# Performance work log

Measured on AMD Instinct MI355X. Metric: run time of the kernel, lower is better.

Reference implementation:

```python
import jax, jax.numpy as jnp
import numpy as np

C0 = 0.28209479177387814
C1 = 0.4886025119029199
C2 = (1.0925484305920792, -1.0925484305920792, 0.31539156525252005,
      -1.0925484305920792, 0.5462742152960396)
EPS = 1e-6


def eval_sh_bases2(d):
    # d: [..., 3] unit directions -> [..., 9] SH basis (degree 2, svox2 convention)
    x, y, z = d[..., 0], d[..., 1], d[..., 2]
    return jnp.stack([
        jnp.full_like(x, C0),
        -C1 * y, C1 * z, -C1 * x,
        C2[0] * x * y, C2[1] * y * z,
        C2[2] * (2.0 * z * z - x * x - y * y),
        C2[3] * x * z, C2[4] * (x * x - y * y),
    ], axis=-1)


def get_sh_vals(xyz, sh_feats, invs, locs):
    # xyz: [N,3]; sh_feats: [J,9]; invs: [J,4,4]; locs: [J,3] -> weights [N,J]
    n = xyz.shape[0]
    xyz_h = jnp.concatenate([xyz, jnp.ones((n, 1), xyz.dtype)], axis=-1)  # [N,4]
    pts = jnp.einsum('jab,nb->jna', invs, xyz_h)[..., :3]  # [J,N,3]
    vd = locs[:, None, :] - pts                             # [J,N,3]
    norm = jnp.linalg.norm(vd, axis=-1)                     # [J,N]
    lengths = jnp.nan_to_num(norm)
    vd = vd / jnp.maximum(norm, 1e-12)[..., None]           # F.normalize
    sh = eval_sh_bases2(vd)                                 # [J,N,9]
    rads = jax.nn.relu(jnp.einsum('jnk,jk->jn', sh, sh_feats) + 0.5)
    rel = jax.nn.relu(1.0 - lengths / jnp.maximum(rads, EPS))
    rel = jnp.where(rads < EPS, 0.0, rel)
    return rel.T  # [N,J]


def weighted_transformation(pts, weights, transforms):
    # pts: [M,3]; weights: [M,J]; transforms: [J,4,4] (already inverse transforms,
    # if_transform_is_inv=True). Linear-blend the matrices and apply.
    wsum = weights.sum(axis=-1, keepdims=True)              # [M,1]
    wn = weights / jnp.maximum(wsum, EPS)
    T = jnp.einsum('mj,jab->mab', wn, transforms)           # [M,4,4]
    p_h = jnp.concatenate([pts, jnp.ones((pts.shape[0], 1), pts.dtype)], axis=-1)
    out = jnp.einsum('mab,mb->ma', T, p_h)[:, :3]
    return jnp.where(wsum > EPS, out, pts)                  # untouched if no weight


def setup_inputs() -> dict:
    key = jax.random.key(0)
    ks = jax.random.split(key, 5)
    B, S, J = 4096, 128, 24
    return {
        'xyz_sampled': jax.random.normal(ks[0], (B, S, 3), jnp.float32),
        'viewdirs': jax.random.normal(ks[1], (B, S, 3), jnp.float32),
        'transforms': jax.random.normal(ks[2], (J, 4, 4), jnp.float32),
        'ray_valid': jnp.ones((B, S), dtype=bool),
        'sh_feats': jax.random.normal(ks[3], (J, 9), jnp.float32),
        'locs': jax.random.normal(ks[4], (J, 3), jnp.float32),
    }


def reference(xyz_sampled, viewdirs, transforms, ray_valid, sh_feats, locs):
    shape = xyz_sampled.shape
    x = xyz_sampled.reshape(-1, 3)
    n = x.shape[0]
    tmp = jnp.concatenate([x, (xyz_sampled - viewdirs).reshape(-1, 3)], axis=0)  # [2N,3]
    w = get_sh_vals(x, sh_feats, transforms, locs)          # [N,J]
    w2 = jnp.concatenate([w, w], axis=0)                    # [2N,J]
    tmp = weighted_transformation(tmp, w2, transforms)      # [2N,3]
    xyz_out = tmp[:n]
    view_out = xyz_out - tmp[n:]
    return xyz_out.reshape(shape), view_out.reshape(shape)
```

## Files before the change

### kernel.cpp

```cpp
#include <hip/hip_runtime.h>

#define EPS 1e-6f
#define J 24


__global__ __launch_bounds__(256, 4) void shcaster_kernel(
    const float* __restrict__ xyz,
    const float* __restrict__ vdir,
    const float* __restrict__ transforms,
    const float* __restrict__ sh_feats,
    const float* __restrict__ locs,
    float* __restrict__ out,
    int n)
{
    __shared__ float4 sj[J][7];
    const int tid = threadIdx.x;

    if (tid < J) {
        const int j = tid;
        float F[9];
        #pragma unroll
        for (int k = 0; k < 9; ++k) F[k] = sh_feats[j * 9 + k];

        const float C0  = 0.28209479177387814f;
        const float C1  = 0.4886025119029199f;
        const float C2a = 1.0925484305920792f;

        const float f0  = C0 * F[0] + 0.5f;
        const float cy  = -C1 * F[1];
        const float cz  =  C1 * F[2];
        const float cx  = -C1 * F[3];
        const float cxy =  C2a * F[4];
        const float cyz = -C2a * F[5];
        const float c6  = 0.31539156525252005f * F[6];
        const float cxz = -C2a * F[7];
        const float c8  = 0.5462742152960396f  * F[8];

        float* s = (float*)&sj[j][0];
        #pragma unroll
        for (int k = 0; k < 12; ++k) s[k] = transforms[j * 16 + k];
        s[12] = locs[j * 3 + 0];
        s[13] = locs[j * 3 + 1];
        s[14] = locs[j * 3 + 2];
        s[15] = f0;
        s[16] = cx;  s[17] = cy;  s[18] = cz;  s[19] = cxy;
        s[20] = cyz; s[21] = cxz;
        s[22] = c8 - c6;
        s[23] = -c6 - c8;
        s[24] = 2.0f * c6;
        s[25] = 0.f; s[26] = 0.f; s[27] = 0.f;
    }
    __syncthreads();

    const int i = blockIdx.x * blockDim.x + tid;
    if (i >= n) return;

    const float px = xyz[3 * i + 0];
    const float py = xyz[3 * i + 1];
    const float pz = xyz[3 * i + 2];
    const float vx = vdir[3 * i + 0];
    const float vy = vdir[3 * i + 1];
    const float vz = vdir[3 * i + 2];

    float wsum = 0.f;
    float Ta[12];
    #pragma unroll
    for (int k = 0; k < 12; ++k) Ta[k] = 0.f;

    #pragma unroll 4
    for (int j = 0; j < J; ++j) {
        const float4 q0 = sj[j][0];
        const float4 q1 = sj[j][1];
        const float4 q2 = sj[j][2];
        const float4 q3 = sj[j][3];
        const float4 q4 = sj[j][4];
        const float4 q5 = sj[j][5];
        const float4 q6 = sj[j][6];

        const float ax = fmaf(q0.x, px, fmaf(q0.y, py, fmaf(q0.z, pz, q0.w)));
        const float ay = fmaf(q1.x, px, fmaf(q1.y, py, fmaf(q1.z, pz, q1.w)));
        const float az = fmaf(q2.x, px, fmaf(q2.y, py, fmaf(q2.z, pz, q2.w)));

        const float dx = q3.x - ax;
        const float dy = q3.y - ay;
        const float dz = q3.z - az;
        const float d2 = fmaf(dx, dx, fmaf(dy, dy, dz * dz));

        const float inv_n = __builtin_amdgcn_rsqf(fmaxf(d2, 1e-24f));
        const float len = d2 * inv_n;
        const float nx = dx * inv_n;
        const float ny = dy * inv_n;
        const float nz = dz * inv_n;

        float rads = q3.w;
        rads = fmaf(q4.x, nx, rads);
        rads = fmaf(q4.y, ny, rads);
        rads = fmaf(q4.z, nz, rads);
        rads = fmaf(q4.w, nx * ny, rads);
        rads = fmaf(q5.x, ny * nz, rads);
        rads = fmaf(q5.y, nx * nz, rads);
        rads = fmaf(q5.z, nx * nx, rads);
        rads = fmaf(q5.w, ny * ny, rads);
        rads = fmaf(q6.x, nz * nz, rads);
        rads = fmaxf(rads, 0.f);

        float rel = fmaxf(1.f - len * __builtin_amdgcn_rcpf(fmaxf(rads, EPS)), 0.f);
        rel = (rads < EPS) ? 0.f : rel;

        wsum += rel;
        Ta[0]  = fmaf(rel, q0.x, Ta[0]);
        Ta[1]  = fmaf(rel, q0.y, Ta[1]);
        Ta[2]  = fmaf(rel, q0.z, Ta[2]);
        Ta[3]  = fmaf(rel, q0.w, Ta[3]);
        Ta[4]  = fmaf(rel, q1.x, Ta[4]);
        Ta[5]  = fmaf(rel, q1.y, Ta[5]);
        Ta[6]  = fmaf(rel, q1.z, Ta[6]);
        Ta[7]  = fmaf(rel, q1.w, Ta[7]);
        Ta[8]  = fmaf(rel, q2.x, Ta[8]);
        Ta[9]  = fmaf(rel, q2.y, Ta[9]);
        Ta[10] = fmaf(rel, q2.z, Ta[10]);
        Ta[11] = fmaf(rel, q2.w, Ta[11]);
    }

    const float inv_w = __builtin_amdgcn_rcpf(fmaxf(wsum, EPS));
    const bool valid = wsum > EPS;

    const float axo = fmaf(Ta[0], px, fmaf(Ta[1], py, fmaf(Ta[2],  pz, Ta[3])))  * inv_w;
    const float ayo = fmaf(Ta[4], px, fmaf(Ta[5], py, fmaf(Ta[6],  pz, Ta[7])))  * inv_w;
    const float azo = fmaf(Ta[8], px, fmaf(Ta[9], py, fmaf(Ta[10], pz, Ta[11]))) * inv_w;

    const float qx = px - vx;
    const float qy = py - vy;
    const float qz = pz - vz;
    const float bxo = fmaf(Ta[0], qx, fmaf(Ta[1], qy, fmaf(Ta[2],  qz, Ta[3])))  * inv_w;
    const float byo = fmaf(Ta[4], qx, fmaf(Ta[5], qy, fmaf(Ta[6],  qz, Ta[7])))  * inv_w;
    const float bzo = fmaf(Ta[8], qx, fmaf(Ta[9], qy, fmaf(Ta[10], qz, Ta[11]))) * inv_w;

    const float ox = valid ? axo : px;
    const float oy = valid ? ayo : py;
    const float oz = valid ? azo : pz;
    const float wx = ox - (valid ? bxo : qx);
    const float wy = oy - (valid ? byo : qy);
    const float wz = oz - (valid ? bzo : qz);

    out[3 * i + 0] = ox;
    out[3 * i + 1] = oy;
    out[3 * i + 2] = oz;
    float* out2 = out + (size_t)3 * n;
    out2[3 * i + 0] = wx;
    out2[3 * i + 1] = wy;
    out2[3 * i + 2] = wz;
}

extern "C" void kernel_launch(void* const* d_in, const int* in_sizes, int n_in,
                              void* d_out, int out_size, void* d_ws, size_t ws_size,
                              hipStream_t stream) {
    const int n = (out_size > 0) ? (out_size / 6) : 524288;
    const int big = 3 * n;

    const float* xyz  = nullptr;
    const float* vdir = nullptr;
    const float* trf  = nullptr;
    const float* shf  = nullptr;
    const float* locs = nullptr;
    int bigSeen = 0;
    for (int k = 0; k < n_in; ++k) {
        const int s = in_sizes[k];
        if (s == big) {
            if (bigSeen++ == 0) xyz = (const float*)d_in[k];
            else                vdir = (const float*)d_in[k];
        } else if (s == 384) {
            trf = (const float*)d_in[k];
        } else if (s == 216) {
            shf = (const float*)d_in[k];
        } else if (s == 72) {
            locs = (const float*)d_in[k];
        }
    }
    if (!xyz || !vdir || !trf || !shf || !locs) {
        xyz  = (const float*)d_in[0];
        vdir = (const float*)d_in[1];
        trf  = (const float*)d_in[2];
        shf  = (const float*)d_in[n_in >= 6 ? 4 : 3];
        locs = (const float*)d_in[n_in >= 6 ? 5 : 4];
    }

    float* out = (float*)d_out;
    const int block = 256;
    const int grid = (n + block - 1) / block;
    shcaster_kernel<<<grid, block, 0, stream>>>(xyz, vdir, trf, shf, locs, out, n);
}
```

Before: 89.53 us.

## Precompute per-joint constants in a separate kernel and read them as uniform loads

Moves the per-joint constant folding out of every block into a tiny prologue kernel that writes the folded table to workspace. The main kernel then reads constants through uniform global loads (likely scalar loads into SGPRs) instead of LDS. It also drops the syncthreads, fully unrolls the joint loop and raises the occupancy hint. This adds a second launch and depends on the scalar cache, and the full unroll may raise register pressure.

Result: slower. 92.09 us (+2.9%).

```diff
diff --git a/kernel.cpp b/kernel.cpp
--- a/kernel.cpp
+++ b/kernel.cpp
@@ -3,56 +3,55 @@
 #define EPS 1e-6f
 #define J 24
 
+__global__ void fold_kernel(const float* __restrict__ transforms,
+                            const float* __restrict__ sh_feats,
+                            const float* __restrict__ locs,
+                            float* __restrict__ cj)
+{
+    const int j = threadIdx.x;
+    if (j >= J) return;
 
-__global__ __launch_bounds__(256, 4) void shcaster_kernel(
+    float F[9];
+    #pragma unroll
+    for (int k = 0; k < 9; ++k) F[k] = sh_feats[j * 9 + k];
+
+    const float C0  = 0.28209479177387814f;
+    const float C1  = 0.4886025119029199f;
+    const float C2a = 1.0925484305920792f;
+
+    const float f0  = C0 * F[0] + 0.5f;
+    const float cy  = -C1 * F[1];
+    const float cz  =  C1 * F[2];
+    const float cx  = -C1 * F[3];
+    const float cxy =  C2a * F[4];
+    const float cyz = -C2a * F[5];
+    const float c6  = 0.31539156525252005f * F[6];
+    const float cxz = -C2a * F[7];
+    const float c8  = 0.5462742152960396f  * F[8];
+
+    float* s = cj + j * 28;
+    #pragma unroll
+    for (int k = 0; k < 12; ++k) s[k] = transforms[j * 16 + k];
+    s[12] = locs[j * 3 + 0];
+    s[13] = locs[j * 3 + 1];
+    s[14] = locs[j * 3 + 2];
+    s[15] = f0;
+    s[16] = cx;  s[17] = cy;  s[18] = cz;
+    s[19] = cxy; s[20] = cyz; s[21] = cxz;
+    s[22] = c8 - c6;
+    s[23] = -c6 - c8;
+    s[24] = 2.0f * c6;
+    s[25] = 0.f; s[26] = 0.f; s[27] = 0.f;
+}
+
+__global__ __launch_bounds__(256, 8) void shcaster_kernel(
     const float* __restrict__ xyz,
     const float* __restrict__ vdir,
-    const float* __restrict__ transforms,
-    const float* __restrict__ sh_feats,
-    const float* __restrict__ locs,
+    const float* __restrict__ cj,
     float* __restrict__ out,
     int n)
 {
-    __shared__ float4 sj[J][7];
-    const int tid = threadIdx.x;
-
-    if (tid < J) {
-        const int j = tid;
-        float F[9];
-        #pragma unroll
-        for (int k = 0; k < 9; ++k) F[k] = sh_feats[j * 9 + k];
-
-        const float C0  = 0.28209479177387814f;
-        const float C1  = 0.4886025119029199f;
-        const float C2a = 1.0925484305920792f;
-
-        const float f0  = C0 * F[0] + 0.5f;
-        const float cy  = -C1 * F[1];
-        const float cz  =  C1 * F[2];
-        const float cx  = -C1 * F[3];
-        const float cxy =  C2a * F[4];
-        const float cyz = -C2a * F[5];
-        const float c6  = 0.31539156525252005f * F[6];
-        const float cxz = -C2a * F[7];
-        const float c8  = 0.5462742152960396f  * F[8];
-
-        float* s = (float*)&sj[j][0];
-        #pragma unroll
-        for (int k = 0; k < 12; ++k) s[k] = transforms[j * 16 + k];
-        s[12] = locs[j * 3 + 0];
-        s[13] = locs[j * 3 + 1];
-        s[14] = locs[j * 3 + 2];
-        s[15] = f0;
-        s[16] = cx;  s[17] = cy;  s[18] = cz;  s[19] = cxy;
-        s[20] = cyz; s[21] = cxz;
-        s[22] = c8 - c6;
-        s[23] = -c6 - c8;
-        s[24] = 2.0f * c6;
-        s[25] = 0.f; s[26] = 0.f; s[27] = 0.f;
-    }
-    __syncthreads();
-
-    const int i = blockIdx.x * blockDim.x + tid;
+    const int i = blockIdx.x * blockDim.x + threadIdx.x;
     if (i >= n) return;
 
     const float px = xyz[3 * i + 0];
@@ -67,23 +66,17 @@
     #pragma unroll
     for (int k = 0; k < 12; ++k) Ta[k] = 0.f;
 
-    #pragma unroll 4
+    #pragma unroll
     for (int j = 0; j < J; ++j) {
-        const float4 q0 = sj[j][0];
-        const float4 q1 = sj[j][1];
-        const float4 q2 = sj[j][2];
-        const float4 q3 = sj[j][3];
-        const float4 q4 = sj[j][4];
-        const float4 q5 = sj[j][5];
-        const float4 q6 = sj[j][6];
+        const float* s = cj + j * 28;
 
-        const float ax = fmaf(q0.x, px, fmaf(q0.y, py, fmaf(q0.z, pz, q0.w)));
-        const float ay = fmaf(q1.x, px, fmaf(q1.y, py, fmaf(q1.z, pz, q1.w)));
-        const float az = fmaf(q2.x, px, fmaf(q2.y, py, fmaf(q2.z, pz, q2.w)));
+        const float ax = fmaf(s[0], px, fmaf(s[1], py, fmaf(s[2],  pz, s[3])));
+        const float ay = fmaf(s[4], px, fmaf(s[5], py, fmaf(s[6],  pz, s[7])));
+        const float az = fmaf(s[8], px, fmaf(s[9], py, fmaf(s[10], pz, s[11])));
 
-        const float dx = q3.x - ax;
-        const float dy = q3.y - ay;
-        const float dz = q3.z - az;
+        const float dx = s[12] - ax;
+        const float dy = s[13] - ay;
+        const float dz = s[14] - az;
         const float d2 = fmaf(dx, dx, fmaf(dy, dy, dz * dz));
 
         const float inv_n = __builtin_amdgcn_rsqf(fmaxf(d2, 1e-24f));
@@ -92,34 +85,34 @@
         const float ny = dy * inv_n;
         const float nz = dz * inv_n;
 
-        float rads = q3.w;
-        rads = fmaf(q4.x, nx, rads);
-        rads = fmaf(q4.y, ny, rads);
-        rads = fmaf(q4.z, nz, rads);
-        rads = fmaf(q4.w, nx * ny, rads);
-        rads = fmaf(q5.x, ny * nz, rads);
-        rads = fmaf(q5.y, nx * nz, rads);
-        rads = fmaf(q5.z, nx * nx, rads);
-        rads = fmaf(q5.w, ny * ny, rads);
-        rads = fmaf(q6.x, nz * nz, rads);
+        float rads = s[15];
+        rads = fmaf(s[16], nx, rads);
+        rads = fmaf(s[17], ny, rads);
+        rads = fmaf(s[18], nz, rads);
+        rads = fmaf(s[19], nx * ny, rads);
+        rads = fmaf(s[20], ny * nz, rads);
+        rads = fmaf(s[21], nx * nz, rads);
+        rads = fmaf(s[22], nx * nx, rads);
+        rads = fmaf(s[23], ny * ny, rads);
+        rads = fmaf(s[24], nz * nz, rads);
         rads = fmaxf(rads, 0.f);
 
         float rel = fmaxf(1.f - len * __builtin_amdgcn_rcpf(fmaxf(rads, EPS)), 0.f);
         rel = (rads < EPS) ? 0.f : rel;
 
         wsum += rel;
-        Ta[0]  = fmaf(rel, q0.x, Ta[0]);
-        Ta[1]  = fmaf(rel, q0.y, Ta[1]);
-        Ta[2]  = fmaf(rel, q0.z, Ta[2]);
-        Ta[3]  = fmaf(rel, q0.w, Ta[3]);
-        Ta[4]  = fmaf(rel, q1.x, Ta[4]);
-        Ta[5]  = fmaf(rel, q1.y, Ta[5]);
-        Ta[6]  = fmaf(rel, q1.z, Ta[6]);
-        Ta[7]  = fmaf(rel, q1.w, Ta[7]);
-        Ta[8]  = fmaf(rel, q2.x, Ta[8]);
-        Ta[9]  = fmaf(rel, q2.y, Ta[9]);
-        Ta[10] = fmaf(rel, q2.z, Ta[10]);
-        Ta[11] = fmaf(rel, q2.w, Ta[11]);
+        Ta[0]  = fmaf(rel, s[0],  Ta[0]);
+        Ta[1]  = fmaf(rel, s[1],  Ta[1]);
+        Ta[2]  = fmaf(rel, s[2],  Ta[2]);
+        Ta[3]  = fmaf(rel, s[3],  Ta[3]);
+        Ta[4]  = fmaf(rel, s[4],  Ta[4]);
+        Ta[5]  = fmaf(rel, s[5],  Ta[5]);
+        Ta[6]  = fmaf(rel, s[6],  Ta[6]);
+        Ta[7]  = fmaf(rel, s[7],  Ta[7]);
+        Ta[8]  = fmaf(rel, s[8],  Ta[8]);
+        Ta[9]  = fmaf(rel, s[9],  Ta[9]);
+        Ta[10] = fmaf(rel, s[10], Ta[10]);
+        Ta[11] = fmaf(rel, s[11], Ta[11]);
     }
 
     const float inv_w = __builtin_amdgcn_rcpf(fmaxf(wsum, EPS));
@@ -185,8 +178,12 @@
         locs = (const float*)d_in[n_in >= 6 ? 5 : 4];
     }
 
+    float* cj = (float*)d_ws;
     float* out = (float*)d_out;
+
+    fold_kernel<<<1, 64, 0, stream>>>(trf, shf, locs, cj);
+
     const int block = 256;
     const int grid = (n + block - 1) / block;
-    shcaster_kernel<<<grid, block, 0, stream>>>(xyz, vdir, trf, shf, locs, out, n);
+    shcaster_kernel<<<grid, block, 0, stream>>>(xyz, vdir, cj, out, n);
 }
```
